# Kernel optimization log

Measured on AMD Instinct MI355X. Metric: run time of the kernel, lower is better.

Reference implementation:

```python
import jax, jax.numpy as jnp
import numpy as np

N = 131072   # n_nodes == n_edges (required by the broadcast in the original module)
C = 256      # node_channels == edge_channels (required by the broadcast)
EPS_BN = 1e-5
EPS = 1e-5


def _linear_params(key, out_c, in_c):
    k1, k2 = jax.random.split(key)
    bound = 1.0 / np.sqrt(in_c)
    W = jax.random.uniform(k1, (out_c, in_c), minval=-bound, maxval=bound, dtype=jnp.float32)
    b = jax.random.uniform(k2, (out_c,), minval=-bound, maxval=bound, dtype=jnp.float32)
    return W, b


def setup_inputs() -> dict:
    key = jax.random.key(0)
    ks = jax.random.split(key, 10)
    h = jax.random.normal(ks[0], (N, C), dtype=jnp.float32)
    e = jax.random.normal(ks[1], (N, C), dtype=jnp.float32)
    edge_index = jax.random.randint(ks[2], (2, N), 0, N, dtype=jnp.int64)
    A_w, A_b = _linear_params(ks[3], C, C)
    B_w, B_b = _linear_params(ks[4], C, C)
    C_w, C_b = _linear_params(ks[5], C, C)
    D_w, D_b = _linear_params(ks[6], C, C)
    U_w, U_b = _linear_params(ks[7], C, C)
    V_w, V_b = _linear_params(ks[8], C, C)
    bn_gamma = jnp.ones((C,), dtype=jnp.float32)
    bn_beta = jnp.zeros((C,), dtype=jnp.float32)
    return dict(h=h, edge_index=edge_index, e=e,
                A_w=A_w, A_b=A_b, B_w=B_w, B_b=B_b,
                C_w=C_w, C_b=C_b, D_w=D_w, D_b=D_b,
                bn_gamma=bn_gamma, bn_beta=bn_beta,
                U_w=U_w, U_b=U_b, V_w=V_w, V_b=V_b)


def reference(h, edge_index, e,
              A_w, A_b, B_w, B_b, C_w, C_b, D_w, D_b,
              bn_gamma, bn_beta, U_w, U_b, V_w, V_b):
    row, col = edge_index[0], edge_index[1]
    # gather + four parallel linears, summed: [E, C]
    e_out = (h[row] @ A_w.T + A_b
             + h[col] @ B_w.T + B_b
             + e[col] @ C_w.T + C_b
             + e[row] @ D_w.T + D_b)
    # BatchNorm1d (training mode: batch stats, biased variance) + ReLU
    mu = jnp.mean(e_out, axis=0)
    var = jnp.var(e_out, axis=0)
    e_out = jax.nn.relu(bn_gamma * (e_out - mu) * jax.lax.rsqrt(var + EPS_BN) + bn_beta)
    # scatter-add edge messages into node-indexed e, then sigmoid-normalize over dim 0
    e_new = e.at[row].add(e_out)
    e_new = jax.nn.sigmoid(e_new)
    e_new = e_new / (jnp.sum(e_new, axis=0, keepdims=True) + EPS)
    # final gather-multiply-reduce: (e_new * V(h[col])).sum(0) broadcasts [N,C]*[E,C] with N==E
    h_out = h @ U_w.T + U_b + jnp.sum(e_new * (h[col] @ V_w.T + V_b), axis=0)
    h_out = jax.nn.relu(h_out)
    return h_out, e_new
```

## Files before the change

### kernel.cpp

```cpp
#include <hip/hip_runtime.h>
#include <hip/hip_bf16.h>


typedef __attribute__((ext_vector_type(8))) short bf16x8;
typedef __attribute__((ext_vector_type(4))) float f32x4;

__device__ __forceinline__ float b2f(unsigned int lo16) {
  union { unsigned int u; float f; } c; c.u = lo16 << 16; return c.f;
}
__device__ __forceinline__ float lof(unsigned int u) { return b2f(u & 0xffffu); }
__device__ __forceinline__ float hif(unsigned int u) { return b2f(u >> 16); }
__device__ __forceinline__ unsigned int f2b(float f) {
  union { float f; unsigned int u; } c; c.f = f;
  unsigned int u = c.u;
  u += 0x7fffu + ((u >> 16) & 1u);
  return u >> 16;
}

__global__ __launch_bounds__(256) void prep_tiled(const float* __restrict__ src,
                                                  unsigned short* __restrict__ dst,
                                                  int nChunks) {
  int g = blockIdx.x * 256 + threadIdx.x;
  if (g >= nChunks) return;
  int mtile = g >> 9;
  int rem = g & 511;
  int r = rem >> 5, k8 = rem & 31;
  const float4* s = reinterpret_cast<const float4*>(src + (((size_t)mtile * 16 + r) << 8) + k8 * 8);
  float4 v0 = s[0], v1 = s[1];
  uint4 o;
  o.x = f2b(v0.x) | (f2b(v0.y) << 16);
  o.y = f2b(v0.z) | (f2b(v0.w) << 16);
  o.z = f2b(v1.x) | (f2b(v1.y) << 16);
  o.w = f2b(v1.z) | (f2b(v1.w) << 16);
  *reinterpret_cast<uint4*>(dst + ((size_t)mtile * 512 + k8 * 16 + r) * 8) = o;
}

__global__ __launch_bounds__(256) void gemm_bt2(
    const unsigned short* __restrict__ Ah, const unsigned short* __restrict__ Ae,
    const unsigned short* __restrict__ Bh, const unsigned short* __restrict__ Be,
    const float* __restrict__ bias, unsigned short* __restrict__ Cmat,
    int O, int nColBlk, int ktSteps, int nBlk) {
  __shared__ char lds[16384];
  const int cpx = nBlk >> 3;
  const int hw = blockIdx.x;
  const int bid = (hw % 8) * cpx + hw / 8;
  const int colBlk = bid % nColBlk;
  const int rowBlk = bid / nColBlk;
  const int tid = threadIdx.x;
  const int w = tid >> 6, lane = tid & 63;
  const int wm = w >> 1, wn = w & 1;

  const size_t aTileOff = (size_t)(rowBlk * 8 + w * 2) * 8192 + lane * 16;
  const size_t bTileOff = (size_t)(colBlk * 8 + w * 2) * 8192 + lane * 16;
  char* ldsA0 = lds + (w * 2) * 1024;
  char* ldsA1 = lds + (w * 2 + 1) * 1024;
  char* ldsB0 = lds + 8192 + (w * 2) * 1024;
  char* ldsB1 = lds + 8192 + (w * 2 + 1) * 1024;

  f32x4 acc[4][4] = {};

  for (int kt = 0; kt < ktSteps; ++kt) {
    const char* Abase = (const char*)(kt < 8 ? Ah : Ae) + aTileOff + (size_t)(kt & 7) * 1024;
    const char* Bbase = (const char*)(kt < 8 ? Bh : Be) + bTileOff + (size_t)(kt & 7) * 1024;
    __builtin_amdgcn_global_load_lds((const __attribute__((address_space(1))) void*)Abase,
                                     (__attribute__((address_space(3))) void*)ldsA0, 16, 0, 0);
    __builtin_amdgcn_global_load_lds((const __attribute__((address_space(1))) void*)(Abase + 8192),
                                     (__attribute__((address_space(3))) void*)ldsA1, 16, 0, 0);
    __builtin_amdgcn_global_load_lds((const __attribute__((address_space(1))) void*)Bbase,
                                     (__attribute__((address_space(3))) void*)ldsB0, 16, 0, 0);
    __builtin_amdgcn_global_load_lds((const __attribute__((address_space(1))) void*)(Bbase + 8192),
                                     (__attribute__((address_space(3))) void*)ldsB1, 16, 0, 0);
    __syncthreads();
    bf16x8 a[4], b[4];
#pragma unroll
    for (int mi = 0; mi < 4; ++mi)
      a[mi] = *reinterpret_cast<const bf16x8*>(lds + (wm * 4 + mi) * 1024 + lane * 16);
#pragma unroll
    for (int ni = 0; ni < 4; ++ni)
      b[ni] = *reinterpret_cast<const bf16x8*>(lds + 8192 + (wn * 4 + ni) * 1024 + lane * 16);
#pragma unroll
    for (int mi = 0; mi < 4; ++mi)
#pragma unroll
      for (int ni = 0; ni < 4; ++ni)
        acc[mi][ni] = __builtin_amdgcn_mfma_f32_16x16x32_bf16(a[mi], b[ni], acc[mi][ni], 0, 0, 0);
    __syncthreads();
  }

  const int rb = rowBlk * 128 + wm * 64 + ((lane >> 4) << 2);
  const int cb = colBlk * 128 + wn * 64 + (lane & 15);
#pragma unroll
  for (int mi = 0; mi < 4; ++mi) {
#pragma unroll
    for (int ni = 0; ni < 4; ++ni) {
      const int coln = cb + ni * 16;
      const float bz = bias[coln];
      const size_t base = (size_t)(rb + mi * 16) * O + coln;
#pragma unroll
      for (int r = 0; r < 4; ++r)
        Cmat[base + (size_t)r * O] = (unsigned short)f2b(acc[mi][ni][r] + bz);
    }
  }
}

__global__ __launch_bounds__(256) void edge_stats(
    const unsigned short* __restrict__ PRPC,
    const int* __restrict__ rows_s, const int* __restrict__ cols_s,
    float* __restrict__ sums, float* __restrict__ sumsq) {
  __shared__ float red[8][256];
  const int c8 = threadIdx.x & 31;
  const int sub = threadIdx.x >> 5;
  float s[8], q[8];
#pragma unroll
  for (int j = 0; j < 8; ++j) { s[j] = 0.f; q[j] = 0.f; }
#pragma unroll 1
  for (int it = 0; it < 8; ++it) {
    const int p = blockIdx.x * 64 + it * 8 + sub;
    const int r = rows_s[p], cj = cols_s[p];
    const uint4 pr = *reinterpret_cast<const uint4*>(PRPC + (size_t)r * 512 + c8 * 8);
    const uint4 pc = *reinterpret_cast<const uint4*>(PRPC + (size_t)cj * 512 + 256 + c8 * 8);
    const unsigned int rw[4] = {pr.x, pr.y, pr.z, pr.w};
    const unsigned int cw[4] = {pc.x, pc.y, pc.z, pc.w};
#pragma unroll
    for (int p4 = 0; p4 < 4; ++p4) {
      const float v0 = lof(rw[p4]) + lof(cw[p4]);
      const float v1 = hif(rw[p4]) + hif(cw[p4]);
      s[2 * p4] += v0;     q[2 * p4] += v0 * v0;
      s[2 * p4 + 1] += v1; q[2 * p4 + 1] += v1 * v1;
    }
  }
#pragma unroll
  for (int j = 0; j < 8; ++j) red[sub][c8 * 8 + j] = s[j];
  __syncthreads();
  {
    const int c = threadIdx.x;
    float t = 0.f;
#pragma unroll
    for (int u2 = 0; u2 < 8; ++u2) t += red[u2][c];
    atomicAdd(sums + c, t);
  }
  __syncthreads();
#pragma unroll
  for (int j = 0; j < 8; ++j) red[sub][c8 * 8 + j] = q[j];
  __syncthreads();
  {
    const int c = threadIdx.x;
    float t = 0.f;
#pragma unroll
    for (int u2 = 0; u2 < 8; ++u2) t += red[u2][c];
    atomicAdd(sumsq + c, t);
  }
}

__global__ void bn_finalize(const float* __restrict__ sums, const float* __restrict__ sumsq,
                            const float* __restrict__ gamma, const float* __restrict__ beta,
                            float* __restrict__ scale, float* __restrict__ shift, float invE) {
  const int c = threadIdx.x;
  const float mu = sums[c] * invE;
  const float var = fmaxf(sumsq[c] * invE - mu * mu, 0.f);
  const float sc = gamma[c] * rsqrtf(var + 1e-5f);
  scale[c] = sc;
  shift[c] = beta[c] - mu * sc;
}

__global__ __launch_bounds__(256) void hist_rows(const int* __restrict__ ei,
                                                 const int* __restrict__ modep,
                                                 int* __restrict__ cnt, int Nn) {
  const int k = blockIdx.x * 256 + threadIdx.x;
  if (k >= Nn) return;
  const int row = (*modep) ? ei[2 * k] : ei[k];
  atomicAdd(&cnt[row], 1);
}

__global__ __launch_bounds__(256) void scan1(const int* __restrict__ cnt,
                                             int* __restrict__ bsum) {
  __shared__ int red[256];
  const int t = threadIdx.x;
  red[t] = cnt[blockIdx.x * 256 + t];
  __syncthreads();
#pragma unroll
  for (int s = 128; s > 0; s >>= 1) {
    if (t < s) red[t] += red[t + s];
    __syncthreads();
  }
  if (t == 0) bsum[blockIdx.x] = red[0];
}

__global__ __launch_bounds__(512) void scan2(int* __restrict__ bsum, int nb) {
  __shared__ int tmp[512];
  const int t = threadIdx.x;
  const int own = (t < nb) ? bsum[t] : 0;
  tmp[t] = own;
  __syncthreads();
  for (int off = 1; off < 512; off <<= 1) {
    int v = (t >= off) ? tmp[t - off] : 0;
    __syncthreads();
    tmp[t] += v;
    __syncthreads();
  }
  if (t < nb) bsum[t] = tmp[t] - own;
}

__global__ __launch_bounds__(256) void scan3(const int* __restrict__ cnt,
                                             const int* __restrict__ bsum,
                                             int* __restrict__ base, int Nn) {
  __shared__ int tmp[256];
  const int t = threadIdx.x;
  const int gid = blockIdx.x * 256 + t;
  const int own = cnt[gid];
  tmp[t] = own;
  __syncthreads();
  for (int off = 1; off < 256; off <<= 1) {
    int v = (t >= off) ? tmp[t - off] : 0;
    __syncthreads();
    tmp[t] += v;
    __syncthreads();
  }
  base[gid] = tmp[t] - own + bsum[blockIdx.x];
  if (gid == 0) base[Nn] = Nn;
}

__global__ __launch_bounds__(256) void scatter_eids(const int* __restrict__ ei,
                                                    const int* __restrict__ modep,
                                                    const int* __restrict__ base,
                                                    int* __restrict__ cnt,
                                                    int* __restrict__ rows_s,
                                                    int* __restrict__ cols_s, int Nn) {
  const int k = blockIdx.x * 256 + threadIdx.x;
  if (k >= Nn) return;
  int row, col;
  if (*modep) { row = ei[2 * k]; col = ei[2 * (Nn + k)]; }
  else        { row = ei[k];     col = ei[Nn + k]; }
  const int pos = base[row] + atomicAdd(&cnt[row], -1) - 1;
  rows_s[pos] = row;
  cols_s[pos] = col;
}

__global__ __launch_bounds__(256) void gather_sig_colsum(
    const float* __restrict__ e, const unsigned short* __restrict__ PRPC,
    const int* __restrict__ base, const int* __restrict__ cols_s,
    const float* __restrict__ scale, const float* __restrict__ shift,
    float* __restrict__ acc, float* __restrict__ colsum) {
  __shared__ float red[4][256];
  const int lane = threadIdx.x & 63, w = threadIdx.x >> 6;
  const float4 sc = *reinterpret_cast<const float4*>(scale + lane * 4);
  const float4 sh = *reinterpret_cast<const float4*>(shift + lane * 4);
  float s0 = 0.f, s1 = 0.f, s2 = 0.f, s3 = 0.f;
  const int n0 = blockIdx.x * 64 + w * 16;
#pragma unroll 1
  for (int it = 0; it < 16; ++it) {
    const int i = n0 + it;
    float4 v = *reinterpret_cast<const float4*>(e + (size_t)i * 256 + lane * 4);
    const uint2 pr = *reinterpret_cast<const uint2*>(PRPC + (size_t)i * 512 + lane * 4);
    const float pr0 = lof(pr.x), pr1 = hif(pr.x), pr2 = lof(pr.y), pr3 = hif(pr.y);
    const int p0 = base[i], p1 = base[i + 1];
#pragma unroll 1
    for (int p = p0; p < p1; ++p) {
      const int cj = cols_s[p];
      const uint2 pc = *reinterpret_cast<const uint2*>(PRPC + (size_t)cj * 512 + 256 + lane * 4);
      v.x += fmaxf(fmaf(sc.x, pr0 + lof(pc.x), sh.x), 0.f);
      v.y += fmaxf(fmaf(sc.y, pr1 + hif(pc.x), sh.y), 0.f);
      v.z += fmaxf(fmaf(sc.z, pr2 + lof(pc.y), sh.z), 0.f);
      v.w += fmaxf(fmaf(sc.w, pr3 + hif(pc.y), sh.w), 0.f);
    }
    v.x = 1.f / (1.f + __expf(-v.x));
    v.y = 1.f / (1.f + __expf(-v.y));
    v.z = 1.f / (1.f + __expf(-v.z));
    v.w = 1.f / (1.f + __expf(-v.w));
    *reinterpret_cast<float4*>(acc + (size_t)i * 256 + lane * 4) = v;
    s0 += v.x; s1 += v.y; s2 += v.z; s3 += v.w;
  }
  red[w][lane * 4 + 0] = s0;
  red[w][lane * 4 + 1] = s1;
  red[w][lane * 4 + 2] = s2;
  red[w][lane * 4 + 3] = s3;
  __syncthreads();
  const int c = threadIdx.x;
  atomicAdd(colsum + c, red[0][c] + red[1][c] + red[2][c] + red[3][c]);
}

__global__ void inv_finalize(const float* __restrict__ colsum, float* __restrict__ inv) {
  const int c = threadIdx.x;
  inv[c] = 1.0f / (colsum[c] + 1e-5f);
}

__global__ __launch_bounds__(256) void enew_T(
    const float* __restrict__ acc, const float* __restrict__ inv,
    const int* __restrict__ ei, const int* __restrict__ modep,
    const unsigned short* __restrict__ VU,
    float* __restrict__ outE, float* __restrict__ T, int Nn) {
  __shared__ float red[8][256];
  const int c8 = threadIdx.x & 31, sub = threadIdx.x >> 5;
  const int mode = *modep;
  float iv[8];
#pragma unroll
  for (int j = 0; j < 8; ++j) iv[j] = inv[c8 * 8 + j];
  float t[8];
#pragma unroll
  for (int j = 0; j < 8; ++j) t[j] = 0.f;
#pragma unroll 1
  for (int it = 0; it < 8; ++it) {
    const int k = blockIdx.x * 64 + it * 8 + sub;
    const int col = mode ? ei[2 * (Nn + k)] : ei[Nn + k];
    const float4* p0 = reinterpret_cast<const float4*>(acc + (size_t)k * 256 + c8 * 8);
    const float4 a = p0[0], b = p0[1];
    float en[8] = {a.x * iv[0], a.y * iv[1], a.z * iv[2], a.w * iv[3],
                   b.x * iv[4], b.y * iv[5], b.z * iv[6], b.w * iv[7]};
    float4 o0, o1;
    o0.x = en[0]; o0.y = en[1]; o0.z = en[2]; o0.w = en[3];
    o1.x = en[4]; o1.y = en[5]; o1.z = en[6]; o1.w = en[7];
    float4* q0 = reinterpret_cast<float4*>(outE + (size_t)k * 256 + c8 * 8);
    q0[0] = o0; q0[1] = o1;
    const uint4 hv = *reinterpret_cast<const uint4*>(VU + (size_t)col * 512 + c8 * 8);
    const unsigned int w4[4] = {hv.x, hv.y, hv.z, hv.w};
#pragma unroll
    for (int p = 0; p < 4; ++p) {
      t[2 * p] += en[2 * p] * lof(w4[p]);
      t[2 * p + 1] += en[2 * p + 1] * hif(w4[p]);
    }
  }
#pragma unroll
  for (int j = 0; j < 8; ++j) red[sub][c8 * 8 + j] = t[j];
  __syncthreads();
  {
    const int c = threadIdx.x;
    float tt = 0.f;
#pragma unroll
    for (int u2 = 0; u2 < 8; ++u2) tt += red[u2][c];
    atomicAdd(T + c, tt);
  }
}

__global__ __launch_bounds__(256) void hout_k(
    const unsigned short* __restrict__ VU, const float* __restrict__ T,
    float* __restrict__ outH, int nChunks) {
  const int g = blockIdx.x * 256 + threadIdx.x;
  if (g >= nChunks) return;
  const int i = g >> 5, c8 = g & 31;
  const uint4 hu = *reinterpret_cast<const uint4*>(VU + (size_t)i * 512 + 256 + c8 * 8);
  const float4 t0 = *reinterpret_cast<const float4*>(T + c8 * 8);
  const float4 t1 = *reinterpret_cast<const float4*>(T + c8 * 8 + 4);
  float4 o0, o1;
  o0.x = fmaxf(lof(hu.x) + t0.x, 0.f);
  o0.y = fmaxf(hif(hu.x) + t0.y, 0.f);
  o0.z = fmaxf(lof(hu.y) + t0.z, 0.f);
  o0.w = fmaxf(hif(hu.y) + t0.w, 0.f);
  o1.x = fmaxf(lof(hu.z) + t1.x, 0.f);
  o1.y = fmaxf(hif(hu.z) + t1.y, 0.f);
  o1.z = fmaxf(lof(hu.w) + t1.z, 0.f);
  o1.w = fmaxf(hif(hu.w) + t1.w, 0.f);
  float4* q = reinterpret_cast<float4*>(outH + (size_t)i * 256 + c8 * 8);
  q[0] = o0; q[1] = o1;
}

__global__ void pack_bias2(const float* a, const float* d, const float* b, const float* cc,
                           const float* v, const float* u,
                           float* b1, float* b2) {
  const int t = threadIdx.x;
  b1[t] = a[t] + d[t];
  b1[256 + t] = b[t] + cc[t];
  b2[t] = v[t];
  b2[256 + t] = u[t];
}

__global__ void detect_idx(const int* __restrict__ ei, int* __restrict__ mode) {
  if (threadIdx.x == 0 && blockIdx.x == 0) {
    int m = 0;
#pragma unroll
    for (int i = 1; i < 64; i += 2) m |= ei[i];
    *mode = (m == 0) ? 1 : 0;
  }
}

extern "C" void kernel_launch(void* const* d_in, const int* in_sizes, int n_in,
                              void* d_out, int out_size, void* d_ws, size_t ws_size,
                              hipStream_t stream) {
  const float* h     = (const float*)d_in[0];
  const int*   ei    = (const int*)d_in[1];
  const float* e     = (const float*)d_in[2];
  const float* Aw    = (const float*)d_in[3];
  const float* Ab    = (const float*)d_in[4];
  const float* Bw    = (const float*)d_in[5];
  const float* Bb    = (const float*)d_in[6];
  const float* Cw    = (const float*)d_in[7];
  const float* Cb    = (const float*)d_in[8];
  const float* Dw    = (const float*)d_in[9];
  const float* Db    = (const float*)d_in[10];
  const float* gamma = (const float*)d_in[11];
  const float* beta  = (const float*)d_in[12];
  const float* Uw    = (const float*)d_in[13];
  const float* Ub    = (const float*)d_in[14];
  const float* Vw    = (const float*)d_in[15];
  const float* Vb    = (const float*)d_in[16];
  const int N = in_sizes[0] / 256;

  char* ws = (char*)d_ws;
  unsigned short* W1h = (unsigned short*)(ws + 0x0);
  unsigned short* W1e = (unsigned short*)(ws + 0x40000);
  unsigned short* W2t = (unsigned short*)(ws + 0x80000);
  float* b1     = (float*)(ws + 0xC0000);
  float* b2     = (float*)(ws + 0xC0800);
  float* sums   = (float*)(ws + 0xC1000);
  float* sumsq  = (float*)(ws + 0xC1400);
  float* colsum = (float*)(ws + 0xC1800);
  float* Tacc   = (float*)(ws + 0xC1C00);
  float* scale  = (float*)(ws + 0xC2000);
  float* shift  = (float*)(ws + 0xC2400);
  float* inv    = (float*)(ws + 0xC2800);
  int*   mode   = (int*)(ws + 0xC2C00);
  unsigned short* h_t  = (unsigned short*)(ws + 0x100000);
  unsigned short* e_t  = (unsigned short*)(ws + 0x4100000);
  unsigned short* PRPC = (unsigned short*)(ws + 0x8100000);
  unsigned short* VU   = (unsigned short*)(ws + 0x10100000);
  float*          acc  = (float*)(ws + 0x100000);
  int* cnt    = (int*)(ws + 0x18100000);
  int* baseA  = (int*)(ws + 0x18180000);
  int* rows_s = (int*)(ws + 0x18210000);
  int* cols_s = (int*)(ws + 0x18290000);
  int* bsum   = (int*)(ws + 0x18310000);

  float* outH = (float*)d_out;
  float* outE = outH + (size_t)N * 256;

  hipMemsetAsync(ws + 0xC1000, 0, 4096, stream);
  hipMemsetAsync(cnt, 0, (size_t)N * 4, stream);
  detect_idx<<<1, 64, 0, stream>>>(ei, mode);
  pack_bias2<<<1, 256, 0, stream>>>(Ab, Db, Bb, Cb, Vb, Ub, b1, b2);
  prep_tiled<<<32, 256, 0, stream>>>(Aw, W1h, 8192);
  prep_tiled<<<32, 256, 0, stream>>>(Bw, W1h + 16 * 4096, 8192);
  prep_tiled<<<32, 256, 0, stream>>>(Dw, W1e, 8192);
  prep_tiled<<<32, 256, 0, stream>>>(Cw, W1e + 16 * 4096, 8192);
  prep_tiled<<<32, 256, 0, stream>>>(Vw, W2t, 8192);
  prep_tiled<<<32, 256, 0, stream>>>(Uw, W2t + 16 * 4096, 8192);

  hist_rows<<<N / 256, 256, 0, stream>>>(ei, mode, cnt, N);
  scan1<<<N / 256 / 256 * 256 + ((N / 256) % 256 ? 1 : 0) + 511, 256, 0, stream>>>(cnt, bsum);
  scan2<<<1, 512, 0, stream>>>(bsum, N / 256);
  scan3<<<N / 256, 256, 0, stream>>>(cnt, bsum, baseA, N);
  scatter_eids<<<N / 256, 256, 0, stream>>>(ei, mode, baseA, cnt, rows_s, cols_s, N);

  const int nChunks = N * 32;
  prep_tiled<<<nChunks / 256, 256, 0, stream>>>(h, h_t, nChunks);
  prep_tiled<<<nChunks / 256, 256, 0, stream>>>(e, e_t, nChunks);
  gemm_bt2<<<(N / 128) * 4, 256, 0, stream>>>(h_t, e_t, W1h, W1e, b1, PRPC, 512, 4, 16, (N / 128) * 4);
  gemm_bt2<<<(N / 128) * 4, 256, 0, stream>>>(h_t, h_t, W2t, W2t, b2, VU, 512, 4, 8, (N / 128) * 4);

  edge_stats<<<N / 64, 256, 0, stream>>>(PRPC, rows_s, cols_s, sums, sumsq);
  bn_finalize<<<1, 256, 0, stream>>>(sums, sumsq, gamma, beta, scale, shift, 1.0f / (float)N);
  gather_sig_colsum<<<N / 64, 256, 0, stream>>>(e, PRPC, baseA, cols_s, scale, shift, acc, colsum);
  inv_finalize<<<1, 256, 0, stream>>>(colsum, inv);
  enew_T<<<N / 64, 256, 0, stream>>>(acc, inv, ei, mode, VU, outE, Tacc, N);
  hout_k<<<nChunks / 256, 256, 0, stream>>>(VU, Tacc, outH, nChunks);
}
```

Before: 639.4 us.

## Merge small launches, fold finalize kernels, and prefetch gathers in edge kernels

Merges the six weight-conversion launches into one kernel and the h/e conversions into one. Removes the separate BN and inverse-colsum finalize kernels by computing them inline in the consumers. Shrinks the oversized scan1 grid. Adds memory-level parallelism to edge_stats and enew_T by batching four gathers per thread, and to gather_sig_colsum by staging column indices in LDS and software-prefetching the next row and next neighbour. The risks are redundant per-block finalize arithmetic and higher register pressure.

```diff
diff --git a/kernel.cpp b/kernel.cpp
--- a/kernel.cpp
+++ b/kernel.cpp
@@ -17,11 +17,8 @@
   return u >> 16;
 }
 
-__global__ __launch_bounds__(256) void prep_tiled(const float* __restrict__ src,
-                                                  unsigned short* __restrict__ dst,
-                                                  int nChunks) {
-  int g = blockIdx.x * 256 + threadIdx.x;
-  if (g >= nChunks) return;
+__device__ __forceinline__ void prep_chunk(const float* __restrict__ src,
+                                           unsigned short* __restrict__ dst, int g) {
   int mtile = g >> 9;
   int rem = g & 511;
   int r = rem >> 5, k8 = rem & 31;
@@ -33,6 +30,37 @@
   o.z = f2b(v1.x) | (f2b(v1.y) << 16);
   o.w = f2b(v1.z) | (f2b(v1.w) << 16);
   *reinterpret_cast<uint4*>(dst + ((size_t)mtile * 512 + k8 * 16 + r) * 8) = o;
+}
+
+__global__ __launch_bounds__(256) void prep_he(const float* __restrict__ h,
+                                               unsigned short* __restrict__ h_t,
+                                               const float* __restrict__ e,
+                                               unsigned short* __restrict__ e_t,
+                                               int nChunksEach) {
+  int g = blockIdx.x * 256 + threadIdx.x;
+  if (g < nChunksEach) prep_chunk(h, h_t, g);
+  else if (g < 2 * nChunksEach) prep_chunk(e, e_t, g - nChunksEach);
+}
+
+__global__ __launch_bounds__(256) void prep_weights(
+    const float* __restrict__ s0, const float* __restrict__ s1,
+    const float* __restrict__ s2, const float* __restrict__ s3,
+    const float* __restrict__ s4, const float* __restrict__ s5,
+    unsigned short* __restrict__ W1h, unsigned short* __restrict__ W1e,
+    unsigned short* __restrict__ W2t) {
+  int g = blockIdx.x * 256 + threadIdx.x;
+  int sel = g >> 13;
+  int gg = g & 8191;
+  const float* src; unsigned short* dst;
+  switch (sel) {
+    case 0: src = s0; dst = W1h; break;
+    case 1: src = s1; dst = W1h + 65536; break;
+    case 2: src = s2; dst = W1e; break;
+    case 3: src = s3; dst = W1e + 65536; break;
+    case 4: src = s4; dst = W2t; break;
+    default: src = s5; dst = W2t + 65536; break;
+  }
+  prep_chunk(src, dst, gg);
 }
 
 __global__ __launch_bounds__(256) void gemm_bt2(
@@ -113,19 +141,29 @@
 #pragma unroll
   for (int j = 0; j < 8; ++j) { s[j] = 0.f; q[j] = 0.f; }
 #pragma unroll 1
-  for (int it = 0; it < 8; ++it) {
-    const int p = blockIdx.x * 64 + it * 8 + sub;
-    const int r = rows_s[p], cj = cols_s[p];
-    const uint4 pr = *reinterpret_cast<const uint4*>(PRPC + (size_t)r * 512 + c8 * 8);
-    const uint4 pc = *reinterpret_cast<const uint4*>(PRPC + (size_t)cj * 512 + 256 + c8 * 8);
-    const unsigned int rw[4] = {pr.x, pr.y, pr.z, pr.w};
-    const unsigned int cw[4] = {pc.x, pc.y, pc.z, pc.w};
-#pragma unroll
-    for (int p4 = 0; p4 < 4; ++p4) {
-      const float v0 = lof(rw[p4]) + lof(cw[p4]);
-      const float v1 = hif(rw[p4]) + hif(cw[p4]);
-      s[2 * p4] += v0;     q[2 * p4] += v0 * v0;
-      s[2 * p4 + 1] += v1; q[2 * p4 + 1] += v1 * v1;
+  for (int grp = 0; grp < 2; ++grp) {
+    const int kb = blockIdx.x * 64 + grp * 32 + sub * 4;
+    int r[4], cj[4];
+#pragma unroll
+    for (int u = 0; u < 4; ++u) { r[u] = rows_s[kb + u]; cj[u] = cols_s[kb + u]; }
+    uint4 pr[4], pc[4];
+#pragma unroll
+    for (int u = 0; u < 4; ++u)
+      pr[u] = *reinterpret_cast<const uint4*>(PRPC + (size_t)r[u] * 512 + c8 * 8);
+#pragma unroll
+    for (int u = 0; u < 4; ++u)
+      pc[u] = *reinterpret_cast<const uint4*>(PRPC + (size_t)cj[u] * 512 + 256 + c8 * 8);
+#pragma unroll
+    for (int u = 0; u < 4; ++u) {
+      const unsigned int rw[4] = {pr[u].x, pr[u].y, pr[u].z, pr[u].w};
+      const unsigned int cw[4] = {pc[u].x, pc[u].y, pc[u].z, pc[u].w};
+#pragma unroll
+      for (int p4 = 0; p4 < 4; ++p4) {
+        const float v0 = lof(rw[p4]) + lof(cw[p4]);
+        const float v1 = hif(rw[p4]) + hif(cw[p4]);
+        s[2 * p4] += v0;     q[2 * p4] += v0 * v0;
+        s[2 * p4 + 1] += v1; q[2 * p4 + 1] += v1 * v1;
+      }
     }
   }
 #pragma unroll
@@ -149,17 +187,6 @@
     for (int u2 = 0; u2 < 8; ++u2) t += red[u2][c];
     atomicAdd(sumsq + c, t);
   }
-}
-
-__global__ void bn_finalize(const float* __restrict__ sums, const float* __restrict__ sumsq,
-                            const float* __restrict__ gamma, const float* __restrict__ beta,
-                            float* __restrict__ scale, float* __restrict__ shift, float invE) {
-  const int c = threadIdx.x;
-  const float mu = sums[c] * invE;
-  const float var = fmaxf(sumsq[c] * invE - mu * mu, 0.f);
-  const float sc = gamma[c] * rsqrtf(var + 1e-5f);
-  scale[c] = sc;
-  shift[c] = beta[c] - mu * sc;
 }
 
 __global__ __launch_bounds__(256) void hist_rows(const int* __restrict__ ei,
@@ -235,38 +262,81 @@
   cols_s[pos] = col;
 }
 
+#define GCAP 1024
 __global__ __launch_bounds__(256) void gather_sig_colsum(
     const float* __restrict__ e, const unsigned short* __restrict__ PRPC,
     const int* __restrict__ base, const int* __restrict__ cols_s,
-    const float* __restrict__ scale, const float* __restrict__ shift,
-    float* __restrict__ acc, float* __restrict__ colsum) {
+    const float* __restrict__ sums, const float* __restrict__ sumsq,
+    const float* __restrict__ gamma, const float* __restrict__ beta,
+    float* __restrict__ acc, float* __restrict__ colsum, float invE) {
   __shared__ float red[4][256];
+  __shared__ int colsL[GCAP];
+  __shared__ int baseL[65];
   const int lane = threadIdx.x & 63, w = threadIdx.x >> 6;
-  const float4 sc = *reinterpret_cast<const float4*>(scale + lane * 4);
-  const float4 sh = *reinterpret_cast<const float4*>(shift + lane * 4);
+  const int n0 = blockIdx.x * 64;
+  if (threadIdx.x < 65) baseL[threadIdx.x] = base[n0 + threadIdx.x];
+  __syncthreads();
+  const int bstart = baseL[0];
+  const int bcount = baseL[64] - bstart;
+  for (int qq = threadIdx.x; qq < bcount && qq < GCAP; qq += 256)
+    colsL[qq] = cols_s[bstart + qq];
+  const float4 sm = *reinterpret_cast<const float4*>(sums + lane * 4);
+  const float4 sq = *reinterpret_cast<const float4*>(sumsq + lane * 4);
+  const float4 gm = *reinterpret_cast<const float4*>(gamma + lane * 4);
+  const float4 bt = *reinterpret_cast<const float4*>(beta + lane * 4);
+  float4 sc, sh;
+  {
+    const float mx = sm.x * invE, my = sm.y * invE, mz = sm.z * invE, mw = sm.w * invE;
+    sc.x = gm.x * rsqrtf(fmaxf(sq.x * invE - mx * mx, 0.f) + 1e-5f);
+    sc.y = gm.y * rsqrtf(fmaxf(sq.y * invE - my * my, 0.f) + 1e-5f);
+    sc.z = gm.z * rsqrtf(fmaxf(sq.z * invE - mz * mz, 0.f) + 1e-5f);
+    sc.w = gm.w * rsqrtf(fmaxf(sq.w * invE - mw * mw, 0.f) + 1e-5f);
+    sh.x = bt.x - mx * sc.x; sh.y = bt.y - my * sc.y;
+    sh.z = bt.z - mz * sc.z; sh.w = bt.w - mw * sc.w;
+  }
+  __syncthreads();
   float s0 = 0.f, s1 = 0.f, s2 = 0.f, s3 = 0.f;
-  const int n0 = blockIdx.x * 64 + w * 16;
+  const int i0 = n0 + w * 16;
+  int p = baseL[w * 16];
+  const int pendW = baseL[w * 16 + 16];
+  uint2 pcn;
+  pcn.x = 0; pcn.y = 0;
+  if (p < pendW) {
+    const int q0 = p - bstart;
+    const int cj = (q0 < GCAP) ? colsL[q0] : cols_s[p];
+    pcn = *reinterpret_cast<const uint2*>(PRPC + (size_t)cj * 512 + 256 + lane * 4);
+  }
+  float4 ev = *reinterpret_cast<const float4*>(e + (size_t)i0 * 256 + lane * 4);
+  uint2 prv = *reinterpret_cast<const uint2*>(PRPC + (size_t)i0 * 512 + lane * 4);
 #pragma unroll 1
   for (int it = 0; it < 16; ++it) {
-    const int i = n0 + it;
-    float4 v = *reinterpret_cast<const float4*>(e + (size_t)i * 256 + lane * 4);
-    const uint2 pr = *reinterpret_cast<const uint2*>(PRPC + (size_t)i * 512 + lane * 4);
+    float4 v = ev;
+    const uint2 pr = prv;
+    if (it + 1 < 16) {
+      ev = *reinterpret_cast<const float4*>(e + (size_t)(i0 + it + 1) * 256 + lane * 4);
+      prv = *reinterpret_cast<const uint2*>(PRPC + (size_t)(i0 + it + 1) * 512 + lane * 4);
+    }
     const float pr0 = lof(pr.x), pr1 = hif(pr.x), pr2 = lof(pr.y), pr3 = hif(pr.y);
-    const int p0 = base[i], p1 = base[i + 1];
+    const int pe = baseL[w * 16 + it + 1];
 #pragma unroll 1
-    for (int p = p0; p < p1; ++p) {
-      const int cj = cols_s[p];
-      const uint2 pc = *reinterpret_cast<const uint2*>(PRPC + (size_t)cj * 512 + 256 + lane * 4);
+    while (p < pe) {
+      const uint2 pc = pcn;
+      if (p + 1 < pendW) {
+        const int qn = p + 1 - bstart;
+        const int cj = (qn < GCAP) ? colsL[qn] : cols_s[p + 1];
+        pcn = *reinterpret_cast<const uint2*>(PRPC + (size_t)cj * 512 + 256 + lane * 4);
+      }
       v.x += fmaxf(fmaf(sc.x, pr0 + lof(pc.x), sh.x), 0.f);
       v.y += fmaxf(fmaf(sc.y, pr1 + hif(pc.x), sh.y), 0.f);
       v.z += fmaxf(fmaf(sc.z, pr2 + lof(pc.y), sh.z), 0.f);
       v.w += fmaxf(fmaf(sc.w, pr3 + hif(pc.y), sh.w), 0.f);
+      ++p;
     }
     v.x = 1.f / (1.f + __expf(-v.x));
     v.y = 1.f / (1.f + __expf(-v.y));
     v.z = 1.f / (1.f + __expf(-v.z));
     v.w = 1.f / (1.f + __expf(-v.w));
-    *reinterpret_cast<float4*>(acc + (size_t)i * 256 + lane * 4) = v;
+    *reinterpret_cast<float4*>(acc + (size_t)(i0 + it) * 256 + lane * 4) = v;
     s0 += v.x; s1 += v.y; s2 += v.z; s3 += v.w;
   }
   red[w][lane * 4 + 0] = s0;
@@ -278,13 +348,8 @@
   atomicAdd(colsum + c, red[0][c] + red[1][c] + red[2][c] + red[3][c]);
 }
 
-__global__ void inv_finalize(const float* __restrict__ colsum, float* __restrict__ inv) {
-  const int c = threadIdx.x;
-  inv[c] = 1.0f / (colsum[c] + 1e-5f);
-}
-
 __global__ __launch_bounds__(256) void enew_T(
-    const float* __restrict__ acc, const float* __restrict__ inv,
+    const float* __restrict__ acc, const float* __restrict__ colsum,
     const int* __restrict__ ei, const int* __restrict__ modep,
     const unsigned short* __restrict__ VU,
     float* __restrict__ outE, float* __restrict__ T, int Nn) {
@@ -293,29 +358,42 @@
   const int mode = *modep;
   float iv[8];
 #pragma unroll
-  for (int j = 0; j < 8; ++j) iv[j] = inv[c8 * 8 + j];
+  for (int j = 0; j < 8; ++j) iv[j] = 1.0f / (colsum[c8 * 8 + j] + 1e-5f);
   float t[8];
 #pragma unroll
   for (int j = 0; j < 8; ++j) t[j] = 0.f;
 #pragma unroll 1
-  for (int it = 0; it < 8; ++it) {
-    const int k = blockIdx.x * 64 + it * 8 + sub;
-    const int col = mode ? ei[2 * (Nn + k)] : ei[Nn + k];
-    const float4* p0 = reinterpret_cast<const float4*>(acc + (size_t)k * 256 + c8 * 8);
-    const float4 a = p0[0], b = p0[1];
-    float en[8] = {a.x * iv[0], a.y * iv[1], a.z * iv[2], a.w * iv[3],
-                   b.x * iv[4], b.y * iv[5], b.z * iv[6], b.w * iv[7]};
-    float4 o0, o1;
-    o0.x = en[0]; o0.y = en[1]; o0.z = en[2]; o0.w = en[3];
-    o1.x = en[4]; o1.y = en[5]; o1.z = en[6]; o1.w = en[7];
-    float4* q0 = reinterpret_cast<float4*>(outE + (size_t)k * 256 + c8 * 8);
-    q0[0] = o0; q0[1] = o1;
-    const uint4 hv = *reinterpret_cast<const uint4*>(VU + (size_t)col * 512 + c8 * 8);
-    const unsigned int w4[4] = {hv.x, hv.y, hv.z, hv.w};
-#pragma unroll
-    for (int p = 0; p < 4; ++p) {
-      t[2 * p] += en[2 * p] * lof(w4[p]);
-      t[2 * p + 1] += en[2 * p + 1] * hif(w4[p]);
+  for (int grp = 0; grp < 2; ++grp) {
+    const int kb = blockIdx.x * 64 + grp * 32 + sub * 4;
+    int col[4];
+#pragma unroll
+    for (int u = 0; u < 4; ++u)
+      col[u] = mode ? ei[2 * (Nn + kb + u)] : ei[Nn + kb + u];
+    uint4 hv[4];
+#pragma unroll
+    for (int u = 0; u < 4; ++u)
+      hv[u] = *reinterpret_cast<const uint4*>(VU + (size_t)col[u] * 512 + c8 * 8);
+    float4 a[4], b[4];
+#pragma unroll
+    for (int u = 0; u < 4; ++u) {
+      const float4* p0 = reinterpret_cast<const float4*>(acc + (size_t)(kb + u) * 256 + c8 * 8);
+      a[u] = p0[0]; b[u] = p0[1];
+    }
+#pragma unroll
+    for (int u = 0; u < 4; ++u) {
+      float en[8] = {a[u].x * iv[0], a[u].y * iv[1], a[u].z * iv[2], a[u].w * iv[3],
+                     b[u].x * iv[4], b[u].y * iv[5], b[u].z * iv[6], b[u].w * iv[7]};
+      float4 o0, o1;
+      o0.x = en[0]; o0.y = en[1]; o0.z = en[2]; o0.w = en[3];
+      o1.x = en[4]; o1.y = en[5]; o1.z = en[6]; o1.w = en[7];
+      float4* q0 = reinterpret_cast<float4*>(outE + (size_t)(kb + u) * 256 + c8 * 8);
+      q0[0] = o0; q0[1] = o1;
+      const unsigned int w4[4] = {hv[u].x, hv[u].y, hv[u].z, hv[u].w};
+#pragma unroll
+      for (int p = 0; p < 4; ++p) {
+        t[2 * p] += en[2 * p] * lof(w4[p]);
+        t[2 * p + 1] += en[2 * p + 1] * hif(w4[p]);
+      }
     }
   }
 #pragma unroll
@@ -403,9 +481,6 @@
   float* sumsq  = (float*)(ws + 0xC1400);
   float* colsum = (float*)(ws + 0xC1800);
   float* Tacc   = (float*)(ws + 0xC1C00);
-  float* scale  = (float*)(ws + 0xC2000);
-  float* shift  = (float*)(ws + 0xC2400);
-  float* inv    = (float*)(ws + 0xC2800);
   int*   mode   = (int*)(ws + 0xC2C00);
   unsigned short* h_t  = (unsigned short*)(ws + 0x100000);
   unsigned short* e_t  = (unsigned short*)(ws + 0x4100000);
@@ -425,29 +500,22 @@
   hipMemsetAsync(cnt, 0, (size_t)N * 4, stream);
   detect_idx<<<1, 64, 0, stream>>>(ei, mode);
   pack_bias2<<<1, 256, 0, stream>>>(Ab, Db, Bb, Cb, Vb, Ub, b1, b2);
-  prep_tiled<<<32, 256, 0, stream>>>(Aw, W1h, 8192);
-  prep_tiled<<<32, 256, 0, stream>>>(Bw, W1h + 16 * 4096, 8192);
-  prep_tiled<<<32, 256, 0, stream>>>(Dw, W1e, 8192);
-  prep_tiled<<<32, 256, 0, stream>>>(Cw, W1e + 16 * 4096, 8192);
-  prep_tiled<<<32, 256, 0, stream>>>(Vw, W2t, 8192);
-  prep_tiled<<<32, 256, 0, stream>>>(Uw, W2t + 16 * 4096, 8192);
+  prep_weights<<<192, 256, 0, stream>>>(Aw, Bw, Dw, Cw, Vw, Uw, W1h, W1e, W2t);
 
   hist_rows<<<N / 256, 256, 0, stream>>>(ei, mode, cnt, N);
-  scan1<<<N / 256 / 256 * 256 + ((N / 256) % 256 ? 1 : 0) + 511, 256, 0, stream>>>(cnt, bsum);
+  scan1<<<N / 256, 256, 0, stream>>>(cnt, bsum);
   scan2<<<1, 512, 0, stream>>>(bsum, N / 256);
   scan3<<<N / 256, 256, 0, stream>>>(cnt, bsum, baseA, N);
   scatter_eids<<<N / 256, 256, 0, stream>>>(ei, mode, baseA, cnt, rows_s, cols_s, N);
 
   const int nChunks = N * 32;
-  prep_tiled<<<nChunks / 256, 256, 0, stream>>>(h, h_t, nChunks);
-  prep_tiled<<<nChunks / 256, 256, 0, stream>>>(e, e_t, nChunks);
+  prep_he<<<2 * nChunks / 256, 256, 0, stream>>>(h, h_t, e, e_t, nChunks);
   gemm_bt2<<<(N / 128) * 4, 256, 0, stream>>>(h_t, e_t, W1h, W1e, b1, PRPC, 512, 4, 16, (N / 128) * 4);
   gemm_bt2<<<(N / 128) * 4, 256, 0, stream>>>(h_t, h_t, W2t, W2t, b2, VU, 512, 4, 8, (N / 128) * 4);
 
   edge_stats<<<N / 64, 256, 0, stream>>>(PRPC, rows_s, cols_s, sums, sumsq);
-  bn_finalize<<<1, 256, 0, stream>>>(sums, sumsq, gamma, beta, scale, shift, 1.0f / (float)N);
-  gather_sig_colsum<<<N / 64, 256, 0, stream>>>(e, PRPC, baseA, cols_s, scale, shift, acc, colsum);
-  inv_finalize<<<1, 256, 0, stream>>>(colsum, inv);
-  enew_T<<<N / 64, 256, 0, stream>>>(acc, inv, ei, mode, VU, outE, Tacc, N);
+  gather_sig_colsum<<<N / 64, 256, 0, stream>>>(e, PRPC, baseA, cols_s, sums, sumsq,
+                                                gamma, beta, acc, colsum, 1.0f / (float)N);
+  enew_T<<<N / 64, 256, 0, stream>>>(acc, colsum, ei, mode, VU, outE, Tacc, N);
   hout_k<<<nChunks / 256, 256, 0, stream>>>(VU, Tacc, outH, nChunks);
 }
```

Result: faster. 607.4 us (-5.0%).
